# Kernel optimization log

Measured on AMD Instinct MI355X. Metric: run time of the kernel, lower is better.

Reference implementation:

```python
import jax, jax.numpy as jnp
import numpy as np
import math

B, S, D, H = 4, 2048, 1024, 16
DK = D // H


def setup_inputs() -> dict:
    key = jax.random.key(0)
    k1, k2, k3, k4, k5 = jax.random.split(key, 5)
    inputs = jax.random.normal(k1, (B, S, D), dtype=jnp.float32)
    # additive causal mask: 0 on/below diagonal, -1e9 above
    causal = jnp.triu(jnp.full((S, S), -1e9, dtype=jnp.float32), k=1)
    mask = causal[None, None, :, :]  # [1,1,S,S]
    w_qkv = jax.random.normal(k2, (D, 3 * D), dtype=jnp.float32) * 0.02
    b_qkv = jax.random.normal(k3, (3 * D,), dtype=jnp.float32) * 0.02
    w_head = jax.random.normal(k4, (D, D), dtype=jnp.float32) * 0.02
    b_head = jax.random.normal(k5, (D,), dtype=jnp.float32) * 0.02
    return {"inputs": inputs, "mask": mask, "w_qkv": w_qkv, "b_qkv": b_qkv,
            "w_head": w_head, "b_head": b_head}


def reference(inputs, mask, w_qkv, b_qkv, w_head, b_head):
    # fused QKV projection
    qkv = jnp.einsum('bsd,de->bse', inputs, w_qkv) + b_qkv  # [B,S,3D]
    q, k, v = jnp.split(qkv, 3, axis=-1)
    # split heads -> [B,H,S,DK]
    q = q.reshape(B, S, H, DK).transpose(0, 2, 1, 3)
    k = k.reshape(B, S, H, DK).transpose(0, 2, 1, 3)
    v = v.reshape(B, S, H, DK).transpose(0, 2, 1, 3)
    # scaled dot-product attention with additive mask
    att = jnp.einsum('bhqd,bhkd->bhqk', q, k) / math.sqrt(DK)
    att = att + mask
    att = jax.nn.softmax(att, axis=-1)  # dropout p=0 -> identity
    out = jnp.einsum('bhqk,bhkd->bhqd', att, v)  # [B,H,S,DK]
    # merge heads
    out = out.transpose(0, 2, 1, 3).reshape(B, S, D)
    out = jnp.einsum('bsd,de->bse', out, w_head) + b_head
    return out
```

## Files before the change

### kernel.cpp

```cpp
#include <hip/hip_runtime.h>
#include <stdint.h>

typedef __bf16 bf16x8 __attribute__((ext_vector_type(8)));
typedef float f32x4 __attribute__((ext_vector_type(4)));
typedef float f32x16 __attribute__((ext_vector_type(16)));
typedef unsigned short u16;

#if __has_builtin(__builtin_amdgcn_exp2f)
#define EXP2F(x) __builtin_amdgcn_exp2f(x)
#else
#define EXP2F(x) exp2f(x)
#endif

__device__ __forceinline__ u16 f2bf(float f) {
  union { float f; unsigned u; } v; v.f = f;
  return (u16)((v.u + 0x7fffu + ((v.u >> 16) & 1u)) >> 16);
}

__device__ __forceinline__ unsigned pk2bf(float a, float b) {
  union { __bf16 h[2]; unsigned u; } c;
  c.h[0] = (__bf16)a; c.h[1] = (__bf16)b;
  return c.u;
}

__device__ __forceinline__ f32x16 vc16(float x) {
  f32x16 v;
#pragma unroll
  for (int i = 0; i < 16; ++i) v[i] = x;
  return v;
}

#define GLOAD_LDS16(gp, lp)                                                       \
  __builtin_amdgcn_global_load_lds((__attribute__((address_space(1))) void*)(gp), \
                                   (__attribute__((address_space(3))) void*)(lp), \
                                   16, 0, 0)

__global__ void k_cvt_bf16(const float* __restrict__ in, u16* __restrict__ out, int n4) {
  int i = blockIdx.x * blockDim.x + threadIdx.x;
  if (i >= n4) return;
  float4 v = ((const float4*)in)[i];
  ushort4 o;
  o.x = f2bf(v.x); o.y = f2bf(v.y); o.z = f2bf(v.z); o.w = f2bf(v.w);
  ((ushort4*)out)[i] = o;
}

__global__ void k_transpose_bf16(const float* __restrict__ w, u16* __restrict__ wt,
                                 int K, int N) {
  __shared__ u16 t[32][33];
  int n0 = blockIdx.x * 32, k0 = blockIdx.y * 32;
  int tx = threadIdx.x & 31, ty = threadIdx.x >> 5;
#pragma unroll
  for (int j = 0; j < 4; ++j) {
    int r = ty + j * 8;
    t[r][tx] = f2bf(w[(size_t)(k0 + r) * N + n0 + tx]);
  }
  __syncthreads();
#pragma unroll
  for (int j = 0; j < 4; ++j) {
    int r = ty + j * 8;
    wt[(size_t)(n0 + r) * K + k0 + tx] = t[tx][r];
  }
}

template <int MODE>
__global__ void __launch_bounds__(256, 2)
k_gemm_bt(const u16* __restrict__ A, const u16* __restrict__ Bt,
          const float* __restrict__ bias, u16* __restrict__ outQ,
          u16* __restrict__ outK, u16* __restrict__ outVt,
          float* __restrict__ outF, int Kdim, int Ncols) {
  __shared__ u16 Asq[128 * 64];
  __shared__ u16 Bsq[128 * 64];
  const int tid = threadIdx.x;
  const int lane = tid & 63;
  const int wv = tid >> 6;
  const int g = lane >> 4;
  const int lr = lane & 15;
  const int wr = wv >> 1, wc = wv & 1;
  const int row0 = blockIdx.y * 128;
  const int col0 = blockIdx.x * 128;

  const f32x4 fzero = {0.f, 0.f, 0.f, 0.f};
  f32x4 acc[4][4];
#pragma unroll
  for (int m = 0; m < 4; ++m)
#pragma unroll
    for (int n = 0; n < 4; ++n) acc[m][n] = fzero;

  const u16* Arow = A + (size_t)row0 * Kdim;
  const u16* Brow = Bt + (size_t)col0 * Kdim;

  for (int kt = 0; kt < Kdim; kt += 64) {
#pragma unroll
    for (int j = 0; j < 4; ++j) {
      int unit = j * 256 + wv * 64 + lane;
      int r = unit >> 3, u = unit & 7;
      int ug = u ^ (r & 7);
      GLOAD_LDS16(Arow + (size_t)r * Kdim + kt + ug * 8,
                  &Asq[(size_t)(j * 256 + wv * 64) * 8]);
      GLOAD_LDS16(Brow + (size_t)r * Kdim + kt + ug * 8,
                  &Bsq[(size_t)(j * 256 + wv * 64) * 8]);
    }
    __syncthreads();
#pragma unroll
    for (int kc = 0; kc < 2; ++kc) {
      bf16x8 af[4], bfr[4];
#pragma unroll
      for (int m = 0; m < 4; ++m) {
        int r = wr * 64 + m * 16 + lr;
        int u = (kc * 4 + g) ^ (r & 7);
        af[m] = *(const bf16x8*)((const char*)Asq + r * 128 + u * 16);
      }
#pragma unroll
      for (int n = 0; n < 4; ++n) {
        int r = wc * 64 + n * 16 + lr;
        int u = (kc * 4 + g) ^ (r & 7);
        bfr[n] = *(const bf16x8*)((const char*)Bsq + r * 128 + u * 16);
      }
#pragma unroll
      for (int m = 0; m < 4; ++m)
#pragma unroll
        for (int n = 0; n < 4; ++n)
          acc[m][n] = __builtin_amdgcn_mfma_f32_16x16x32_bf16(af[m], bfr[n],
                                                              acc[m][n], 0, 0, 0);
    }
    __syncthreads();
  }

#pragma unroll
  for (int n = 0; n < 4; ++n) {
    int e = col0 + wc * 64 + n * 16 + lr;
    float bv = bias[e];
    if (MODE == 0) {
      int part = e >> 10;
      int d = e & 1023;
      int hh = d >> 6;
      int dk = d & 63;
#pragma unroll
      for (int m = 0; m < 4; ++m) {
        int tbase = row0 + wr * 64 + m * 16 + g * 4;
        int bb = tbase >> 11;
        int s = tbase & 2047;
        size_t bh = (size_t)((bb << 4) + hh);
        if (part == 2) {
          ushort4 pk;
          pk.x = f2bf(acc[m][n][0] + bv);
          pk.y = f2bf(acc[m][n][1] + bv);
          pk.z = f2bf(acc[m][n][2] + bv);
          pk.w = f2bf(acc[m][n][3] + bv);
          int sp = (s & ~15) | ((g & 1) << 3) | ((g >> 1) << 2);
          *(ushort4*)(outVt + (bh * 64 + dk) * 2048 + sp) = pk;
        } else {
#pragma unroll
          for (int i = 0; i < 4; ++i) {
            float val = acc[m][n][i] + bv;
            size_t off = (bh * 2048 + (size_t)(s + i)) * 64 + dk;
            if (part == 0)
              outQ[off] = f2bf(val * 0.18033688f);
            else
              outK[off] = f2bf(val);
          }
        }
      }
    } else {
#pragma unroll
      for (int m = 0; m < 4; ++m)
#pragma unroll
        for (int i = 0; i < 4; ++i) {
          int t = row0 + wr * 64 + m * 16 + g * 4 + i;
          outF[(size_t)t * Ncols + e] = acc[m][n][i] + bv;
        }
    }
  }
}


__device__ __forceinline__ void stage_kv(const u16* __restrict__ Kb,
                                         const u16* __restrict__ Vb, int kbase,
                                         u16* Kbuf, u16* Vbuf, int wv, int lane) {
#pragma unroll
  for (int j = 0; j < 2; ++j) {
    int unit = j * 256 + wv * 64 + lane;
    int r = unit >> 3, u = unit & 7;
    int ug = u ^ (r & 7);
    GLOAD_LDS16(Kb + (size_t)(kbase + r) * 64 + ug * 8, Kbuf + (j * 256 + wv * 64) * 8);
    GLOAD_LDS16(Vb + (size_t)r * 2048 + kbase + ug * 8, Vbuf + (j * 256 + wv * 64) * 8);
  }
}

__global__ void __launch_bounds__(256, 4)
k_flash(const u16* __restrict__ Qg, const u16* __restrict__ Kg,
        const u16* __restrict__ Vtg, u16* __restrict__ attn,
        float* __restrict__ outP, float* __restrict__ mlb) {
  __shared__ u16 KV[2][2][4096];
  const int tid = threadIdx.x;
  const int lane = tid & 63;
  const int wv = tid >> 6;
  const int ql = lane & 31;
  const int hi = lane >> 5;

  const int T_QB[24] = {15,15,7, 14,14, 13,13,6, 12,12, 11,11,5, 10,10, 9,9,4, 8,8, 3,2,1,0};
  const int T_KS[24] = { 0,16,0,  0,15,  0,14,0,  0,13,  0,12,0,  0,11, 0,10,0, 0,9, 0,0,0,0};
  const int T_KC[24] = {16,16,16,15,15, 14,14,14, 13,13, 12,12,12,11,11,10,10,10,9,9, 8,6,4,2};
  const int T_MD[24] = { 1, 2,0,  1, 2,  1, 2,0,  1, 2,  1, 2,0,  1, 2, 1, 2,0, 1,2, 0,0,0,0};

  const int bid = blockIdx.x;
  const int g2 = bid >> 6;
  const int bh = bid & 63;
  const int qb = T_QB[g2];
  const int ks = T_KS[g2];
  const int kcnt = T_KC[g2];
  const int md = T_MD[g2];

  const u16* Qb = Qg + (size_t)bh * 2048 * 64;
  const u16* Kb = Kg + (size_t)bh * 2048 * 64;
  const u16* Vb = Vtg + (size_t)bh * 64 * 2048;
  const int bb = bh >> 4, hh = bh & 15;

  int off[4];
#pragma unroll
  for (int j = 0; j < 4; ++j) off[j] = ql * 64 + (((2 * j + hi) ^ (ql & 7)) * 8);

  const int q0w = qb * 128 + wv * 32;
  const int q = q0w + ql;

  bf16x8 qf[4];
#pragma unroll
  for (int ds = 0; ds < 4; ++ds)
    qf[ds] = *(const bf16x8*)(Qb + (size_t)q * 64 + ds * 16 + hi * 8);

  f32x16 o0 = vc16(0.f), o1 = vc16(0.f);
  float lrow = 0.f;

  stage_kv(Kb, Vb, ks * 64, &KV[0][0][0], &KV[0][1][0], wv, lane);
  __syncthreads();

  for (int it = 0; it < kcnt; ++it) {
    const int kbase = (ks + it) * 64;
    const int nb = it & 1;
    if (it + 1 < kcnt)
      stage_kv(Kb, Vb, kbase + 64, &KV[nb ^ 1][0][0], &KV[nb ^ 1][1][0], wv, lane);
    const u16* Kbuf = &KV[nb][0][0];
    const u16* Vbuf = &KV[nb][1][0];

    if (kbase <= q0w + 31) {
      const bool need1 = (kbase + 32) <= (q0w + 31);
      f32x16 s0 = vc16(-4.f), s1 = vc16(-4.f);
      __builtin_amdgcn_s_setprio(1);
#pragma unroll
      for (int ds = 0; ds < 4; ++ds) {
        bf16x8 kf = *(const bf16x8*)(Kbuf + off[ds]);
        s0 = __builtin_amdgcn_mfma_f32_32x32x16_bf16(kf, qf[ds], s0, 0, 0, 0);
      }
      if (need1) {
#pragma unroll
        for (int ds = 0; ds < 4; ++ds) {
          bf16x8 kf = *(const bf16x8*)(Kbuf + 2048 + off[ds]);
          s1 = __builtin_amdgcn_mfma_f32_32x32x16_bf16(kf, qf[ds], s1, 0, 0, 0);
        }
      }
      __builtin_amdgcn_s_setprio(0);

      if (kbase + 63 > q0w) {
#pragma unroll
        for (int r = 0; r < 16; ++r) {
          const int krel = (r & 3) + 8 * (r >> 2) + 4 * hi;
          if (kbase + krel > q) s0[r] = -1e30f;
          if (kbase + 32 + krel > q) s1[r] = -1e30f;
        }
      }

#pragma unroll
      for (int r = 0; r < 16; ++r) {
        s0[r] = EXP2F(s0[r]);
        s1[r] = EXP2F(s1[r]);
      }
      float b0[8];
#pragma unroll
      for (int i = 0; i < 8; ++i) b0[i] = (s0[i] + s0[i + 8]) + (s1[i] + s1[i + 8]);
      float b1[4];
#pragma unroll
      for (int i = 0; i < 4; ++i) b1[i] = b0[i] + b0[i + 4];
      float rs = (b1[0] + b1[1]) + (b1[2] + b1[3]);
      rs += __shfl_xor(rs, 32);
      lrow += rs;

      __builtin_amdgcn_s_setprio(1);
#pragma unroll
      for (int kc = 0; kc < 4; ++kc) {
        if (kc < 2 || need1) {
          const int h = kc & 1;
          union { unsigned u[4]; bf16x8 v; } pf;
          if (kc < 2) {
            pf.u[0] = pk2bf(s0[8 * h + 0], s0[8 * h + 1]);
            pf.u[1] = pk2bf(s0[8 * h + 2], s0[8 * h + 3]);
            pf.u[2] = pk2bf(s0[8 * h + 4], s0[8 * h + 5]);
            pf.u[3] = pk2bf(s0[8 * h + 6], s0[8 * h + 7]);
          } else {
            pf.u[0] = pk2bf(s1[8 * h + 0], s1[8 * h + 1]);
            pf.u[1] = pk2bf(s1[8 * h + 2], s1[8 * h + 3]);
            pf.u[2] = pk2bf(s1[8 * h + 4], s1[8 * h + 5]);
            pf.u[3] = pk2bf(s1[8 * h + 6], s1[8 * h + 7]);
          }
          bf16x8 vf0 = *(const bf16x8*)(Vbuf + off[kc]);
          o0 = __builtin_amdgcn_mfma_f32_32x32x16_bf16(vf0, pf.v, o0, 0, 0, 0);
          bf16x8 vf1 = *(const bf16x8*)(Vbuf + 2048 + off[kc]);
          o1 = __builtin_amdgcn_mfma_f32_32x32x16_bf16(vf1, pf.v, o1, 0, 0, 0);
        }
      }
      __builtin_amdgcn_s_setprio(0);
    }
    __syncthreads();
  }

  if (md == 0) {
    const float inv = 1.f / lrow;
    const size_t rowoff = ((size_t)(bb * 2048 + q)) * 1024 + hh * 64;
#pragma unroll
    for (int r4 = 0; r4 < 4; ++r4) {
      ushort4 pa;
      pa.x = f2bf(o0[4 * r4 + 0] * inv);
      pa.y = f2bf(o0[4 * r4 + 1] * inv);
      pa.z = f2bf(o0[4 * r4 + 2] * inv);
      pa.w = f2bf(o0[4 * r4 + 3] * inv);
      *(ushort4*)(attn + rowoff + 8 * r4 + 4 * hi) = pa;
      ushort4 pb;
      pb.x = f2bf(o1[4 * r4 + 0] * inv);
      pb.y = f2bf(o1[4 * r4 + 1] * inv);
      pb.z = f2bf(o1[4 * r4 + 2] * inv);
      pb.w = f2bf(o1[4 * r4 + 3] * inv);
      *(ushort4*)(attn + rowoff + 32 + 8 * r4 + 4 * hi) = pb;
    }
  } else {
    const int pidx = bh * 8 + (qb - 8);
    const int r = wv * 32 + ql;
    float* Op = outP + ((md == 1) ? 0 : 4194304) + (size_t)pidx * 8192 + r * 64;
#pragma unroll
    for (int r4 = 0; r4 < 4; ++r4) {
      float4 pa = {o0[4 * r4 + 0], o0[4 * r4 + 1], o0[4 * r4 + 2], o0[4 * r4 + 3]};
      *(float4*)(Op + 8 * r4 + 4 * hi) = pa;
      float4 pb = {o1[4 * r4 + 0], o1[4 * r4 + 1], o1[4 * r4 + 2], o1[4 * r4 + 3]};
      *(float4*)(Op + 32 + 8 * r4 + 4 * hi) = pb;
    }
    if (hi == 0) mlb[(size_t)pidx * 256 + r * 2 + (md - 1)] = lrow;
  }
}

__global__ void k_combine(const float* __restrict__ Op, const float* __restrict__ mlb,
                          u16* __restrict__ attn) {
  const int pidx = blockIdx.x;
  const int bh = pidx >> 3, qb = 8 + (pidx & 7);
  const int bb = bh >> 4, hh = bh & 15;
  const int tid = threadIdx.x;
  const int dq = (tid & 15) * 4;
  const float* O0 = Op + (size_t)pidx * 8192;
  const float* O1 = O0 + 4194304;
  for (int rb = 0; rb < 128; rb += 16) {
    const int r = rb + (tid >> 4);
    float l0 = mlb[(size_t)pidx * 256 + r * 2];
    float l1 = mlb[(size_t)pidx * 256 + r * 2 + 1];
    float inv = 1.f / (l0 + l1);
    float4 x0 = *(const float4*)(O0 + r * 64 + dq);
    float4 x1 = *(const float4*)(O1 + r * 64 + dq);
    ushort4 o;
    o.x = f2bf((x0.x + x1.x) * inv);
    o.y = f2bf((x0.y + x1.y) * inv);
    o.z = f2bf((x0.z + x1.z) * inv);
    o.w = f2bf((x0.w + x1.w) * inv);
    *(ushort4*)(attn + ((size_t)(bb * 2048 + qb * 128 + r)) * 1024 + hh * 64 + dq) = o;
  }
}

extern "C" void kernel_launch(void* const* d_in, const int* in_sizes, int n_in,
                              void* d_out, int out_size, void* d_ws, size_t ws_size,
                              hipStream_t stream) {
  const float* x      = (const float*)d_in[0];
  const float* w_qkv  = (const float*)d_in[2];
  const float* b_qkv  = (const float*)d_in[3];
  const float* w_head = (const float*)d_in[4];
  const float* b_head = (const float*)d_in[5];
  float* out = (float*)d_out;

  u16* Xb    = (u16*)d_ws;
  u16* Wqkvt = Xb + (size_t)8192 * 1024;
  u16* Wht   = Wqkvt + (size_t)3072 * 1024;
  u16* Qw    = Wht + (size_t)1024 * 1024;
  u16* Kw    = Qw + (size_t)64 * 2048 * 64;
  u16* Vtw   = Kw + (size_t)64 * 2048 * 64;
  u16* Attn  = Xb;
  float* Opart = out;
  float* Mlb   = (float*)Wqkvt;

  k_cvt_bf16<<<8192, 256, 0, stream>>>(x, Xb, (8192 * 1024) / 4);
  k_transpose_bf16<<<dim3(96, 32), 256, 0, stream>>>(w_qkv, Wqkvt, 1024, 3072);
  k_transpose_bf16<<<dim3(32, 32), 256, 0, stream>>>(w_head, Wht, 1024, 1024);
  k_gemm_bt<0><<<dim3(24, 64), 256, 0, stream>>>(Xb, Wqkvt, b_qkv, Qw, Kw, Vtw,
                                                 nullptr, 1024, 3072);
  k_flash<<<1536, 256, 0, stream>>>(Qw, Kw, Vtw, Attn, Opart, Mlb);
  k_combine<<<512, 256, 0, stream>>>(Opart, Mlb, Attn);
  k_gemm_bt<1><<<dim3(8, 64), 256, 0, stream>>>(Attn, Wht, b_head, nullptr, nullptr,
                                                nullptr, out, 1024, 1024);
}
```

Measured before the change: 150.7 us.

## Merge prolog conversion kernels and compute softmax row sums via MFMA with ones

Three preprocessing launches (input bf16 conversion and two weight transposes) become one kernel that dispatches on block index, removing two kernel launches and their gaps. In the flash attention loop, the scalar VALU tree reduction plus cross-lane shuffle for the softmax denominator is replaced by an extra MFMA that multiplies the bf16 probabilities by a ones vector into a third accumulator. This moves work from VALU to the matrix unit but adds one MFMA per chunk and 16 accumulator registers, and the row sum now uses the bf16-rounded probabilities.

Result: slower. 164.5 us (+9.2%).

```diff
diff --git a/kernel.cpp b/kernel.cpp
--- a/kernel.cpp
+++ b/kernel.cpp
@@ -35,20 +35,33 @@
                                    (__attribute__((address_space(3))) void*)(lp), \
                                    16, 0, 0)
 
-__global__ void k_cvt_bf16(const float* __restrict__ in, u16* __restrict__ out, int n4) {
-  int i = blockIdx.x * blockDim.x + threadIdx.x;
-  if (i >= n4) return;
-  float4 v = ((const float4*)in)[i];
-  ushort4 o;
-  o.x = f2bf(v.x); o.y = f2bf(v.y); o.z = f2bf(v.z); o.w = f2bf(v.w);
-  ((ushort4*)out)[i] = o;
-}
-
-__global__ void k_transpose_bf16(const float* __restrict__ w, u16* __restrict__ wt,
-                                 int K, int N) {
+__global__ void k_prolog(const float* __restrict__ x, u16* __restrict__ Xb,
+                         const float* __restrict__ w_qkv, u16* __restrict__ Wqkvt,
+                         const float* __restrict__ w_head, u16* __restrict__ Wht) {
   __shared__ u16 t[32][33];
-  int n0 = blockIdx.x * 32, k0 = blockIdx.y * 32;
-  int tx = threadIdx.x & 31, ty = threadIdx.x >> 5;
+  const int bid = blockIdx.x;
+  const int tid = threadIdx.x;
+  if (bid < 8192) {
+    int i = bid * 256 + tid;
+    float4 v = ((const float4*)x)[i];
+    ushort4 o;
+    o.x = f2bf(v.x); o.y = f2bf(v.y); o.z = f2bf(v.z); o.w = f2bf(v.w);
+    ((ushort4*)Xb)[i] = o;
+    return;
+  }
+  const float* w;
+  u16* wt;
+  int N, bx, by;
+  if (bid < 11264) {
+    w = w_qkv; wt = Wqkvt; N = 3072;
+    bx = (bid - 8192) % 96; by = (bid - 8192) / 96;
+  } else {
+    w = w_head; wt = Wht; N = 1024;
+    bx = (bid - 11264) % 32; by = (bid - 11264) / 32;
+  }
+  const int K = 1024;
+  int n0 = bx * 32, k0 = by * 32;
+  int tx = tid & 31, ty = tid >> 5;
 #pragma unroll
   for (int j = 0; j < 4; ++j) {
     int r = ty + j * 8;
@@ -228,8 +241,11 @@
   for (int ds = 0; ds < 4; ++ds)
     qf[ds] = *(const bf16x8*)(Qb + (size_t)q * 64 + ds * 16 + hi * 8);
 
-  f32x16 o0 = vc16(0.f), o1 = vc16(0.f);
-  float lrow = 0.f;
+  bf16x8 ones;
+#pragma unroll
+  for (int i = 0; i < 8; ++i) ones[i] = (__bf16)1.0f;
+
+  f32x16 o0 = vc16(0.f), o1 = vc16(0.f), o2 = vc16(0.f);
 
   stage_kv(Kb, Vb, ks * 64, &KV[0][0][0], &KV[0][1][0], wv, lane);
   __syncthreads();
@@ -274,37 +290,38 @@
         s0[r] = EXP2F(s0[r]);
         s1[r] = EXP2F(s1[r]);
       }
-      float b0[8];
-#pragma unroll
-      for (int i = 0; i < 8; ++i) b0[i] = (s0[i] + s0[i + 8]) + (s1[i] + s1[i + 8]);
-      float b1[4];
-#pragma unroll
-      for (int i = 0; i < 4; ++i) b1[i] = b0[i] + b0[i + 4];
-      float rs = (b1[0] + b1[1]) + (b1[2] + b1[3]);
-      rs += __shfl_xor(rs, 32);
-      lrow += rs;
-
-      __builtin_amdgcn_s_setprio(1);
+
+      unsigned W[4][4];
 #pragma unroll
       for (int kc = 0; kc < 4; ++kc) {
         if (kc < 2 || need1) {
           const int h = kc & 1;
+          if (kc < 2) {
+            W[kc][0] = pk2bf(s0[8 * h + 0], s0[8 * h + 1]);
+            W[kc][1] = pk2bf(s0[8 * h + 2], s0[8 * h + 3]);
+            W[kc][2] = pk2bf(s0[8 * h + 4], s0[8 * h + 5]);
+            W[kc][3] = pk2bf(s0[8 * h + 6], s0[8 * h + 7]);
+          } else {
+            W[kc][0] = pk2bf(s1[8 * h + 0], s1[8 * h + 1]);
+            W[kc][1] = pk2bf(s1[8 * h + 2], s1[8 * h + 3]);
+            W[kc][2] = pk2bf(s1[8 * h + 4], s1[8 * h + 5]);
+            W[kc][3] = pk2bf(s1[8 * h + 6], s1[8 * h + 7]);
+          }
+        }
+      }
+
+      __builtin_amdgcn_s_setprio(1);
+#pragma unroll
+      for (int kc = 0; kc < 4; ++kc) {
+        if (kc < 2 || need1) {
           union { unsigned u[4]; bf16x8 v; } pf;
-          if (kc < 2) {
-            pf.u[0] = pk2bf(s0[8 * h + 0], s0[8 * h + 1]);
-            pf.u[1] = pk2bf(s0[8 * h + 2], s0[8 * h + 3]);
-            pf.u[2] = pk2bf(s0[8 * h + 4], s0[8 * h + 5]);
-            pf.u[3] = pk2bf(s0[8 * h + 6], s0[8 * h + 7]);
-          } else {
-            pf.u[0] = pk2bf(s1[8 * h + 0], s1[8 * h + 1]);
-            pf.u[1] = pk2bf(s1[8 * h + 2], s1[8 * h + 3]);
-            pf.u[2] = pk2bf(s1[8 * h + 4], s1[8 * h + 5]);
-            pf.u[3] = pk2bf(s1[8 * h + 6], s1[8 * h + 7]);
-          }
+          pf.u[0] = W[kc][0]; pf.u[1] = W[kc][1];
+          pf.u[2] = W[kc][2]; pf.u[3] = W[kc][3];
           bf16x8 vf0 = *(const bf16x8*)(Vbuf + off[kc]);
           o0 = __builtin_amdgcn_mfma_f32_32x32x16_bf16(vf0, pf.v, o0, 0, 0, 0);
           bf16x8 vf1 = *(const bf16x8*)(Vbuf + 2048 + off[kc]);
           o1 = __builtin_amdgcn_mfma_f32_32x32x16_bf16(vf1, pf.v, o1, 0, 0, 0);
+          o2 = __builtin_amdgcn_mfma_f32_32x32x16_bf16(ones, pf.v, o2, 0, 0, 0);
         }
       }
       __builtin_amdgcn_s_setprio(0);
@@ -313,7 +330,7 @@
   }
 
   if (md == 0) {
-    const float inv = 1.f / lrow;
+    const float inv = 1.f / o2[0];
     const size_t rowoff = ((size_t)(bb * 2048 + q)) * 1024 + hh * 64;
 #pragma unroll
     for (int r4 = 0; r4 < 4; ++r4) {
@@ -341,7 +358,7 @@
       float4 pb = {o1[4 * r4 + 0], o1[4 * r4 + 1], o1[4 * r4 + 2], o1[4 * r4 + 3]};
       *(float4*)(Op + 32 + 8 * r4 + 4 * hi) = pb;
     }
-    if (hi == 0) mlb[(size_t)pidx * 256 + r * 2 + (md - 1)] = lrow;
+    if (hi == 0) mlb[(size_t)pidx * 256 + r * 2 + (md - 1)] = o2[0];
   }
 }
 
@@ -390,9 +407,7 @@
   float* Opart = out;
   float* Mlb   = (float*)Wqkvt;
 
-  k_cvt_bf16<<<8192, 256, 0, stream>>>(x, Xb, (8192 * 1024) / 4);
-  k_transpose_bf16<<<dim3(96, 32), 256, 0, stream>>>(w_qkv, Wqkvt, 1024, 3072);
-  k_transpose_bf16<<<dim3(32, 32), 256, 0, stream>>>(w_head, Wht, 1024, 1024);
+  k_prolog<<<12288, 256, 0, stream>>>(x, Xb, w_qkv, Wqkvt, w_head, Wht);
   k_gemm_bt<0><<<dim3(24, 64), 256, 0, stream>>>(Xb, Wqkvt, b_qkv, Qw, Kw, Vtw,
                                                  nullptr, 1024, 3072);
   k_flash<<<1536, 256, 0, stream>>>(Qw, Kw, Vtw, Attn, Opart, Mlb);
```
